# Performance work log

Measured on AMD Instinct MI355X. Metric: run time of the kernel, lower is better.

The kernel has to match this reference:

```python
import jax, jax.numpy as jnp
import numpy as np

E = 512   # embed_size
H = 8     # num_heads
D = E // H
N = 4
T = 2048


def quantize(x, b, e):
    # fake-quant: scale by 2^e, clamp to signed b-bit range, floor, dequant
    s = jnp.exp2(e)
    lo = -jnp.exp2(b - 1.0)
    hi = jnp.exp2(b - 1.0) - 1.0
    return jnp.floor(jnp.clip(x / s, lo, hi)) * s


def setup_inputs() -> dict:
    key = jax.random.key(0)
    ks = jax.random.split(key, 8)
    f = lambda k, shape: jax.random.normal(k, shape, dtype=jnp.float32)
    w = 1.0 / np.sqrt(E)  # ~ torch Linear init scale
    return {
        "values": f(ks[0], (N, T, E)),
        "keys": f(ks[1], (N, T, E)),
        "query": f(ks[2], (N, T, E)),
        "Wq": f(ks[3], (E, E)) * w, "bq": jnp.zeros((E,), jnp.float32),
        "Wk": f(ks[4], (E, E)) * w, "bk": jnp.zeros((E,), jnp.float32),
        "Wv": f(ks[5], (E, E)) * w, "bv": jnp.zeros((E,), jnp.float32),
        "Wo": f(ks[6], (E, E)) * w, "bo": jnp.zeros((E,), jnp.float32),
        "b_param": jnp.float32(8.0),
        "e_param": jnp.float32(0.0),
    }


def reference(values, keys, query, Wq, bq, Wk, bk, Wv, bv, Wo, bo, b_param, e_param):
    n, t, emb = query.shape
    d = emb // H
    # linear projections (torch Linear: x @ W^T + b), split heads -> [N,H,T,D]
    q = (query @ Wq.T + bq).reshape(n, t, H, d).transpose(0, 2, 1, 3)
    k = (keys @ Wk.T + bk).reshape(n, t, H, d).transpose(0, 2, 1, 3)
    v = (values @ Wv.T + bv).reshape(n, t, H, d).transpose(0, 2, 1, 3)
    b = jnp.clip(b_param, 1.0, 8.0)
    q = quantize(q, b, e_param)
    k = quantize(k, b, e_param)
    v = quantize(v, b, e_param)
    # NOTE: source scales by sqrt(embed_size), not sqrt(head_dim)
    energy = jnp.einsum('nhqd,nhkd->nhqk', q, k) / jnp.sqrt(jnp.float32(emb))
    attn = jax.nn.softmax(energy, axis=-1)
    out = jnp.einsum('nhqk,nhkd->nhqd', attn, v)
    out = out.transpose(0, 2, 1, 3).reshape(n, t, emb)
    return out @ Wo.T + bo
```

## Files before the change

kernel.cpp:

```cpp
#include <hip/hip_runtime.h>
#include <hip/hip_bf16.h>
#include <hip/hip_fp16.h>
#include <cstdint>
#include <cstddef>


typedef __attribute__((ext_vector_type(8))) _Float16 f16x8;
typedef __attribute__((ext_vector_type(2))) __fp16 hf16x2;
typedef __attribute__((ext_vector_type(16))) float f32x16;
typedef __attribute__((ext_vector_type(4))) unsigned u32x4;
typedef unsigned short u16;

#define EL  4194304
#define WEL 262144

static __device__ __forceinline__ u16 f2h(float x) {
  _Float16 h = (_Float16)x;
  return __builtin_bit_cast(u16, h);
}
static __device__ __forceinline__ unsigned pkh2(float a, float b) {
  hf16x2 p = __builtin_amdgcn_cvt_pkrtz(a, b);
  return __builtin_bit_cast(unsigned, p);
}
static __device__ __forceinline__ void gl_lds16(const void* g, void* l) {
  __builtin_amdgcn_global_load_lds(
      (__attribute__((address_space(1))) void*)g,
      (__attribute__((address_space(3))) void*)l, 16, 0, 0);
}

struct PrepAllArgs { const float* src[7]; };

__global__ __launch_bounds__(256) void prep_all_kernel(PrepAllArgs a,
                                                       u16* __restrict__ dst)
{
  const int i = blockIdx.x * 256 + threadIdx.x;
  const float* src; int off;
  if (i < 3145728) {
    const int m = i >> 20; off = i & 1048575;
    src = (m == 0) ? a.src[0] : (m == 1) ? a.src[1] : a.src[2];
  } else {
    const int j = i - 3145728; const int w = j >> 16; off = j & 65535;
    src = (w == 0) ? a.src[3] : (w == 1) ? a.src[4]
        : (w == 2) ? a.src[5] : a.src[6];
  }
  const float4 v = ((const float4*)src)[off];
  ushort4 o;
  o.x = f2h(v.x); o.y = f2h(v.y); o.z = f2h(v.z); o.w = f2h(v.w);
  ((ushort4*)dst)[i] = o;
}

struct ProjArgs {
  const u16* X[3]; const u16* W[3]; const float* bias[3];
  u16* dst[3]; int trans[3];
};

__global__ __launch_bounds__(256, 3) void proj_kernel(ProjArgs args,
    const float* __restrict__ bparam, const float* __restrict__ eparam)
{
  __shared__ u16 sm[17408];
  u16* const As = sm;
  u16* const Bs = sm + 8192;

  const int z = blockIdx.z;
  const u16* __restrict__ X = args.X[z];
  const u16* __restrict__ W = args.W[z];
  const float* __restrict__ bias = args.bias[z];
  u16* __restrict__ dst = args.dst[z];
  const int trans = args.trans[z];

  const int tid  = threadIdx.x;
  const int lane = tid & 63;
  const int wave = tid >> 6;
  const int lam  = lane & 31;
  const int hl   = lane >> 5;
  const int wm   = wave & 1;
  const int wn   = wave >> 1;
  const int mbase = blockIdx.x * 128;
  const int nbase = blockIdx.y * 128;

  const int srow = tid >> 3;
  const int sj   = (tid & 7) ^ (srow & 7);
  const u16* gA = X + (size_t)(mbase + srow) * 512 + sj * 8;
  const u16* gB = W + (size_t)(nbase + srow) * 512 + sj * 8;

  int offA[2][4], offB[2][4];
#pragma unroll
  for (int f = 0; f < 2; ++f)
#pragma unroll
    for (int kk = 0; kk < 4; ++kk) {
      const int c = 2 * kk + hl;
      const int m = wm * 64 + f * 32 + lam;
      offA[f][kk] = m * 128 + ((c ^ (m & 7)) * 16);
      const int nn = wn * 64 + f * 32 + lam;
      offB[f][kk] = nn * 128 + ((c ^ (nn & 7)) * 16);
    }

  f32x16 acc[2][2];
#pragma unroll
  for (int a = 0; a < 2; ++a)
#pragma unroll
    for (int b = 0; b < 2; ++b)
#pragma unroll
      for (int i = 0; i < 16; ++i) acc[a][b][i] = 0.f;

  for (int kt = 0; kt < 512; kt += 64) {
    __syncthreads();
#pragma unroll
    for (int t = 0; t < 4; ++t) {
      gl_lds16(gA + kt + t * 32 * 512, (char*)As + tid * 16 + t * 4096);
      gl_lds16(gB + kt + t * 32 * 512, (char*)Bs + tid * 16 + t * 4096);
    }
    __syncthreads();

    f16x8 fA[2][4], fB[2][4];
#pragma unroll
    for (int f = 0; f < 2; ++f)
#pragma unroll
      for (int kk = 0; kk < 4; ++kk) {
        fA[f][kk] = *(const f16x8*)((const char*)As + offA[f][kk]);
        fB[f][kk] = *(const f16x8*)((const char*)Bs + offB[f][kk]);
      }
#pragma unroll
    for (int mf = 0; mf < 2; ++mf)
#pragma unroll
      for (int nf = 0; nf < 2; ++nf)
#pragma unroll
        for (int kk = 0; kk < 4; ++kk)
          acc[mf][nf] = __builtin_amdgcn_mfma_f32_32x32x16_f16(
              fA[mf][kk], fB[nf][kk], acc[mf][nf], 0, 0, 0);
  }

  const float bq   = fminf(fmaxf(bparam[0], 1.0f), 8.0f);
  const float e    = eparam[0];
  const float s    = exp2f(e);
  const float invs = exp2f(-e);
  const float qlo  = -exp2f(bq - 1.0f);
  const float qhi  = exp2f(bq - 1.0f) - 1.0f;
  const int nidx = mbase >> 11;
  const int tb   = mbase & 2047;
  const int hb   = nbase >> 6;

  if (!trans) {
#pragma unroll
    for (int mf = 0; mf < 2; ++mf)
#pragma unroll
      for (int nf = 0; nf < 2; ++nf)
#pragma unroll
        for (int reg = 0; reg < 16; ++reg) {
          int col = wn * 64 + nf * 32 + lam;
          int row = wm * 64 + mf * 32 + (reg & 3) + 8 * (reg >> 2) + 4 * hl;
          float v = acc[mf][nf][reg] + bias[nbase + col];
          float qv = floorf(fminf(fmaxf(v * invs, qlo), qhi)) * s;
          dst[((size_t)(nidx * 8 + hb + (col >> 6)) * 2048 + tb + row) * 64 +
              (col & 63)] = f2h(qv);
        }
  } else {
    __syncthreads();
#pragma unroll
    for (int mf = 0; mf < 2; ++mf)
#pragma unroll
      for (int nf = 0; nf < 2; ++nf)
#pragma unroll
        for (int reg = 0; reg < 16; ++reg) {
          int col = wn * 64 + nf * 32 + lam;
          int row = wm * 64 + mf * 32 + (reg & 3) + 8 * (reg >> 2) + 4 * hl;
          float v = acc[mf][nf][reg] + bias[nbase + col];
          float qv = floorf(fminf(fmaxf(v * invs, qlo), qhi)) * s;
          sm[col * 136 + row] = f2h(qv);
        }
    __syncthreads();
    const int r = tid >> 1, half = tid & 1;
    const u16* sp = sm + r * 136 + half * 64;
    u16* gp = dst + ((size_t)(nidx * 8 + hb + (r >> 6)) * 64 + (r & 63)) * 2048 +
              tb + half * 64;
#pragma unroll
    for (int i = 0; i < 8; ++i)
      *(uint4*)(gp + i * 8) = *(const uint4*)(sp + i * 8);
  }
}

__global__ __launch_bounds__(256, 2) void attn_kernel(
    const u16* __restrict__ qbuf, const u16* __restrict__ kbuf,
    const u16* __restrict__ vtbuf, u16* __restrict__ ctx)
{
  __shared__ u16 sm[35328];
  char* const smc = (char*)sm;

  const int tid  = threadIdx.x;
  const int wave = tid >> 6;
  const int lane = tid & 63;
  const int lam  = lane & 31;
  const int hl   = lane >> 5;
  const int qt = blockIdx.x, hd = blockIdx.y, n = blockIdx.z;
  const int nh = n * 8 + hd;
  const int qbase = qt * 64;

  const u16* Qp = qbuf + ((size_t)nh * 2048 + qbase) * 64;
  const u16* Kp = kbuf + (size_t)nh * 131072;
  const u16* Vp = vtbuf + (size_t)nh * 131072;

  f16x8 qf[2][4];
#pragma unroll
  for (int qb = 0; qb < 2; ++qb)
#pragma unroll
    for (int dk = 0; dk < 4; ++dk)
      qf[qb][dk] = *(const f16x8*)(Qp + (qb * 32 + lam) * 64 + dk * 16 + hl * 8);

  const float sc = (float)(1.4426950408889634 / 22.627416997969522);

  const int r0 = tid >> 3;
  const int j0 = (tid & 7) ^ (r0 & 7);
  const u16* gK0 = Kp + (size_t)r0 * 64 + j0 * 8;
  const u16* gK1 = Kp + (size_t)(r0 + 32) * 64 + j0 * 8;
  const u16* gV0 = Vp + (size_t)r0 * 2048 + j0 * 8;
  const u16* gV1 = Vp + (size_t)(r0 + 32) * 2048 + j0 * 8;

  int offK[2][4], offV[2][4];
#pragma unroll
  for (int kf = 0; kf < 2; ++kf)
#pragma unroll
    for (int dk = 0; dk < 4; ++dk)
      offK[kf][dk] = wave * 8192 + (kf * 32 + lam) * 128 +
                     (((2 * dk + hl) ^ (lam & 7)) * 16);
#pragma unroll
  for (int nf = 0; nf < 2; ++nf)
#pragma unroll
    for (int kk = 0; kk < 4; ++kk)
      offV[nf][kk] = 32768 + wave * 8192 + (nf * 32 + lam) * 128 +
                     (((2 * kk + hl) ^ (lam & 7)) * 16);

  float l_acc[2] = {0.f, 0.f};
  f32x16 O[2][2];
#pragma unroll
  for (int a = 0; a < 2; ++a)
#pragma unroll
    for (int b = 0; b < 2; ++b)
#pragma unroll
      for (int i = 0; i < 16; ++i) O[a][b][i] = 0.f;

  for (int kt = 0; kt < 2048; kt += 256) {
    __syncthreads();
#pragma unroll
    for (int wt = 0; wt < 4; ++wt) {
      const size_t ko = (size_t)(kt + wt * 64) * 64;
      const int    vo = kt + wt * 64;
      gl_lds16(gK0 + ko, smc + wt * 8192 + tid * 16);
      gl_lds16(gK1 + ko, smc + wt * 8192 + tid * 16 + 4096);
      gl_lds16(gV0 + vo, smc + 32768 + wt * 8192 + tid * 16);
      gl_lds16(gV1 + vo, smc + 32768 + wt * 8192 + tid * 16 + 4096);
    }
    __syncthreads();

#pragma unroll
    for (int kf = 0; kf < 2; ++kf) {
      f16x8 Kf[4], Vf[2][2];
#pragma unroll
      for (int dk = 0; dk < 4; ++dk)
        Kf[dk] = *(const f16x8*)(smc + offK[kf][dk]);
#pragma unroll
      for (int nf = 0; nf < 2; ++nf)
#pragma unroll
        for (int kkl = 0; kkl < 2; ++kkl)
          Vf[nf][kkl] = *(const f16x8*)(smc + offV[nf][2 * kf + kkl]);

#pragma unroll
      for (int qb = 0; qb < 2; ++qb) {
        f32x16 S;
#pragma unroll
        for (int i = 0; i < 16; ++i) S[i] = 0.f;
#pragma unroll
        for (int dk = 0; dk < 4; ++dk)
          S = __builtin_amdgcn_mfma_f32_32x32x16_f16(Kf[dk], qf[qb][dk],
                                                     S, 0, 0, 0);
        unsigned pk[4][2];
#pragma unroll
        for (int gh = 0; gh < 4; ++gh) {
          float p0 = __builtin_amdgcn_exp2f(S[4 * gh + 0] * sc);
          float p1 = __builtin_amdgcn_exp2f(S[4 * gh + 1] * sc);
          float p2 = __builtin_amdgcn_exp2f(S[4 * gh + 2] * sc);
          float p3 = __builtin_amdgcn_exp2f(S[4 * gh + 3] * sc);
          l_acc[qb] += (p0 + p1) + (p2 + p3);
          pk[gh][0] = pkh2(p0, p1);
          pk[gh][1] = pkh2(p2, p3);
        }
        f16x8 pfrag[2];
#pragma unroll
        for (int kkl = 0; kkl < 2; ++kkl) {
          unsigned s0 = hl ? pk[2 * kkl][0] : pk[2 * kkl + 1][0];
          unsigned s1 = hl ? pk[2 * kkl][1] : pk[2 * kkl + 1][1];
          unsigned o0 = hl ? pk[2 * kkl + 1][0] : pk[2 * kkl][0];
          unsigned o1 = hl ? pk[2 * kkl + 1][1] : pk[2 * kkl][1];
          unsigned rr0 = (unsigned)__shfl_xor((int)s0, 32);
          unsigned rr1 = (unsigned)__shfl_xor((int)s1, 32);
          u32x4 f;
          f[0] = hl ? rr0 : o0;
          f[1] = hl ? rr1 : o1;
          f[2] = hl ? o0 : rr0;
          f[3] = hl ? o1 : rr1;
          pfrag[kkl] = __builtin_bit_cast(f16x8, f);
        }
#pragma unroll
        for (int nf = 0; nf < 2; ++nf)
#pragma unroll
          for (int kkl = 0; kkl < 2; ++kkl)
            O[qb][nf] = __builtin_amdgcn_mfma_f32_32x32x16_f16(
                pfrag[kkl], Vf[nf][kkl], O[qb][nf], 0, 0, 0);
      }
    }
  }

#pragma unroll
  for (int qb = 0; qb < 2; ++qb) l_acc[qb] += __shfl_xor(l_acc[qb], 32);
  __syncthreads();
  float* lred = (float*)(smc + 69632);
  if (hl == 0) {
    lred[wave * 64 + lam]      = l_acc[0];
    lred[wave * 64 + 32 + lam] = l_acc[1];
  }
  float* Ow = (float*)(smc + wave * 17408);
#pragma unroll
  for (int qb = 0; qb < 2; ++qb)
#pragma unroll
    for (int nf = 0; nf < 2; ++nf)
#pragma unroll
      for (int r = 0; r < 16; ++r) {
        int qrow = qb * 32 + (r & 3) + 8 * (r >> 2) + 4 * hl;
        Ow[qrow * 68 + nf * 32 + lam] = O[qb][nf][r];
      }
  __syncthreads();

  const int q  = tid >> 2;
  const int d4 = (tid & 3) * 64;
  float acc[16];
  {
    const float4 v0 = *(const float4*)(smc + q * 272 + d4);
    const float4 v1 = *(const float4*)(smc + q * 272 + d4 + 16);
    const float4 v2 = *(const float4*)(smc + q * 272 + d4 + 32);
    const float4 v3 = *(const float4*)(smc + q * 272 + d4 + 48);
    acc[0]=v0.x; acc[1]=v0.y; acc[2]=v0.z; acc[3]=v0.w;
    acc[4]=v1.x; acc[5]=v1.y; acc[6]=v1.z; acc[7]=v1.w;
    acc[8]=v2.x; acc[9]=v2.y; acc[10]=v2.z; acc[11]=v2.w;
    acc[12]=v3.x; acc[13]=v3.y; acc[14]=v3.z; acc[15]=v3.w;
  }
#pragma unroll
  for (int w = 1; w < 4; ++w) {
    const char* b = smc + w * 17408 + q * 272 + d4;
    const float4 v0 = *(const float4*)(b);
    const float4 v1 = *(const float4*)(b + 16);
    const float4 v2 = *(const float4*)(b + 32);
    const float4 v3 = *(const float4*)(b + 48);
    acc[0]+=v0.x; acc[1]+=v0.y; acc[2]+=v0.z; acc[3]+=v0.w;
    acc[4]+=v1.x; acc[5]+=v1.y; acc[6]+=v1.z; acc[7]+=v1.w;
    acc[8]+=v2.x; acc[9]+=v2.y; acc[10]+=v2.z; acc[11]+=v2.w;
    acc[12]+=v3.x; acc[13]+=v3.y; acc[14]+=v3.z; acc[15]+=v3.w;
  }
  const float lsum = lred[q] + lred[64 + q] + lred[128 + q] + lred[192 + q];
  const float rinv = 1.0f / lsum;
  unsigned outp[8];
#pragma unroll
  for (int i = 0; i < 8; ++i)
    outp[i] = pkh2(acc[2 * i] * rinv, acc[2 * i + 1] * rinv);
  u16* cp = ctx + ((size_t)n * 2048 + qbase + q) * 512 + hd * 64 + (tid & 3) * 16;
  *(uint4*)cp       = *(const uint4*)&outp[0];
  *(uint4*)(cp + 8) = *(const uint4*)&outp[4];
}

__global__ __launch_bounds__(256) void outproj_kernel(
    const u16* __restrict__ ctxb, const u16* __restrict__ Wof,
    const float* __restrict__ bias, float* __restrict__ out)
{
  __shared__ u16 sm[12288];
  u16* const As = sm;
  u16* const Bs = sm + 4096;

  const int tid  = threadIdx.x;
  const int lane = tid & 63;
  const int wave = tid >> 6;
  const int lam  = lane & 31;
  const int hl   = lane >> 5;
  const int wm   = wave & 1;
  const int wn   = wave >> 1;
  const int mbase = blockIdx.x * 64;
  const int nbase = blockIdx.y * 128;

  const int srow = tid >> 3;
  const int sj   = (tid & 7) ^ (srow & 7);
  const u16* gA = ctxb + (size_t)(mbase + srow) * 512 + sj * 8;
  const u16* gB = Wof  + (size_t)(nbase + srow) * 512 + sj * 8;

  int offA[4], offB[2][4];
#pragma unroll
  for (int kk = 0; kk < 4; ++kk) {
    const int c = 2 * kk + hl;
    const int m = wm * 32 + lam;
    offA[kk] = m * 128 + ((c ^ (m & 7)) * 16);
#pragma unroll
    for (int f = 0; f < 2; ++f) {
      const int nn = wn * 64 + f * 32 + lam;
      offB[f][kk] = nn * 128 + ((c ^ (nn & 7)) * 16);
    }
  }

  f32x16 acc[2];
#pragma unroll
  for (int a = 0; a < 2; ++a)
#pragma unroll
    for (int i = 0; i < 16; ++i) acc[a][i] = 0.f;

  for (int kt = 0; kt < 512; kt += 64) {
    __syncthreads();
#pragma unroll
    for (int t = 0; t < 2; ++t)
      gl_lds16(gA + kt + t * 32 * 512, (char*)As + tid * 16 + t * 4096);
#pragma unroll
    for (int t = 0; t < 4; ++t)
      gl_lds16(gB + kt + t * 32 * 512, (char*)Bs + tid * 16 + t * 4096);
    __syncthreads();

    f16x8 fA[4], fB[2][4];
#pragma unroll
    for (int kk = 0; kk < 4; ++kk) {
      fA[kk] = *(const f16x8*)((const char*)As + offA[kk]);
#pragma unroll
      for (int f = 0; f < 2; ++f)
        fB[f][kk] = *(const f16x8*)((const char*)Bs + offB[f][kk]);
    }
#pragma unroll
    for (int nf = 0; nf < 2; ++nf)
#pragma unroll
      for (int kk = 0; kk < 4; ++kk)
        acc[nf] = __builtin_amdgcn_mfma_f32_32x32x16_f16(
            fA[kk], fB[nf][kk], acc[nf], 0, 0, 0);
  }

#pragma unroll
  for (int nf = 0; nf < 2; ++nf)
#pragma unroll
    for (int reg = 0; reg < 16; ++reg) {
      int col = nbase + wn * 64 + nf * 32 + lam;
      int row = mbase + wm * 32 + (reg & 3) + 8 * (reg >> 2) + 4 * hl;
      out[(size_t)row * 512 + col] = acc[nf][reg] + bias[col];
    }
}

extern "C" void kernel_launch(void* const* d_in, const int* in_sizes, int n_in,
                              void* d_out, int out_size, void* d_ws, size_t ws_size,
                              hipStream_t stream) {
  (void)in_sizes; (void)n_in; (void)out_size; (void)ws_size;
  const float* values = (const float*)d_in[0];
  const float* keys   = (const float*)d_in[1];
  const float* query  = (const float*)d_in[2];
  const float* Wq = (const float*)d_in[3];  const float* bq = (const float*)d_in[4];
  const float* Wk = (const float*)d_in[5];  const float* bk = (const float*)d_in[6];
  const float* Wv = (const float*)d_in[7];  const float* bv = (const float*)d_in[8];
  const float* Wo = (const float*)d_in[9];  const float* bo = (const float*)d_in[10];
  const float* bp = (const float*)d_in[11]; const float* ep = (const float*)d_in[12];

  u16* ws    = (u16*)d_ws;
  u16* qbuf  = ws;
  u16* kbuf  = ws + (size_t)EL;
  u16* vtbuf = ws + (size_t)2 * EL;
  u16* ctx   = ws + (size_t)3 * EL;
  u16* xwf   = ws + (size_t)4 * EL;

  PrepAllArgs pa;
  pa.src[0] = query; pa.src[1] = keys; pa.src[2] = values;
  pa.src[3] = Wq; pa.src[4] = Wk; pa.src[5] = Wv; pa.src[6] = Wo;
  prep_all_kernel<<<13312, 256, 0, stream>>>(pa, xwf);

  const float* Bsrc[3] = {bq, bk, bv};
  u16* Dst[3] = {qbuf, kbuf, vtbuf};
  ProjArgs a;
  for (int m = 0; m < 3; ++m) {
    a.X[m] = xwf + (size_t)m * EL;
    a.W[m] = xwf + (size_t)3 * EL + (size_t)m * WEL;
    a.bias[m] = Bsrc[m]; a.dst[m] = Dst[m]; a.trans[m] = (m == 2);
  }
  proj_kernel<<<dim3(64, 4, 3), 256, 0, stream>>>(a, bp, ep);

  attn_kernel<<<dim3(32, 8, 4), 256, 0, stream>>>(qbuf, kbuf, vtbuf, ctx);
  outproj_kernel<<<dim3(128, 4), 256, 0, stream>>>(
      ctx, xwf + (size_t)3 * EL + (size_t)3 * WEL, bo, (float*)d_out);
}
```

Baseline: 194.2 us.

## Pre-swizzle K/V tiles in projection and pipeline per-wave async loads in attention

The projection kernel now writes K and V^T in a tiled, XOR-swizzled layout that matches the attention kernel's LDS fragment order. Each attention wave can then stream its own contiguous 32-key K/V chunks straight into private LDS with direct global-to-LDS loads. The loads are double-buffered using vmcnt waits instead of block-wide __syncthreads, which removes barrier stalls and overlaps loading with MFMA work. LDS use drops, and the final cross-wave reduction is split into two halves to fit the smaller buffer. The cost is fragile hand-written waitcnt sequencing and a layout coupling between the two kernels.

```diff
diff --git a/kernel.cpp b/kernel.cpp
--- a/kernel.cpp
+++ b/kernel.cpp
@@ -66,7 +66,7 @@
   const u16* __restrict__ W = args.W[z];
   const float* __restrict__ bias = args.bias[z];
   u16* __restrict__ dst = args.dst[z];
-  const int trans = args.trans[z];
+  const int mode = args.trans[z];
 
   const int tid  = threadIdx.x;
   const int lane = tid & 63;
@@ -140,7 +140,7 @@
   const int tb   = mbase & 2047;
   const int hb   = nbase >> 6;
 
-  if (!trans) {
+  if (mode == 0) {
 #pragma unroll
     for (int mf = 0; mf < 2; ++mf)
 #pragma unroll
@@ -154,6 +154,23 @@
           dst[((size_t)(nidx * 8 + hb + (col >> 6)) * 2048 + tb + row) * 64 +
               (col & 63)] = f2h(qv);
         }
+  } else if (mode == 1) {
+#pragma unroll
+    for (int mf = 0; mf < 2; ++mf)
+#pragma unroll
+      for (int nf = 0; nf < 2; ++nf)
+#pragma unroll
+        for (int reg = 0; reg < 16; ++reg) {
+          int col = wn * 64 + nf * 32 + lam;
+          int row = wm * 64 + mf * 32 + (reg & 3) + 8 * (reg >> 2) + 4 * hl;
+          float v = acc[mf][nf][reg] + bias[nbase + col];
+          float qv = floorf(fminf(fmaxf(v * invs, qlo), qhi)) * s;
+          const int t = tb + row;
+          const int d = col & 63;
+          dst[(size_t)(nidx * 8 + hb + (col >> 6)) * 131072 +
+              (t >> 5) * 2048 + (t & 31) * 64 + (((d >> 3) ^ (t & 7)) << 3) +
+              (d & 7)] = f2h(qv);
+        }
   } else {
     __syncthreads();
 #pragma unroll
@@ -171,11 +188,15 @@
     __syncthreads();
     const int r = tid >> 1, half = tid & 1;
     const u16* sp = sm + r * 136 + half * 64;
-    u16* gp = dst + ((size_t)(nidx * 8 + hb + (r >> 6)) * 64 + (r & 63)) * 2048 +
-              tb + half * 64;
-#pragma unroll
-    for (int i = 0; i < 8; ++i)
-      *(uint4*)(gp + i * 8) = *(const uint4*)(sp + i * 8);
+    const int d = r & 63;
+    const int dsw = d & 3;
+    u16* const gp0 = dst + (size_t)(nidx * 8 + hb + (r >> 6)) * 131072;
+#pragma unroll
+    for (int i = 0; i < 8; ++i) {
+      const int t = tb + half * 64 + i * 8;
+      *(uint4*)(gp0 + (t >> 5) * 2048 + d * 32 +
+                ((((t >> 3) & 3) ^ dsw) << 3)) = *(const uint4*)(sp + i * 8);
+    }
   }
 }
 
@@ -183,7 +204,7 @@
     const u16* __restrict__ qbuf, const u16* __restrict__ kbuf,
     const u16* __restrict__ vtbuf, u16* __restrict__ ctx)
 {
-  __shared__ u16 sm[35328];
+  __shared__ u16 sm[25088];
   char* const smc = (char*)sm;
 
   const int tid  = threadIdx.x;
@@ -196,8 +217,9 @@
   const int qbase = qt * 64;
 
   const u16* Qp = qbuf + ((size_t)nh * 2048 + qbase) * 64;
-  const u16* Kp = kbuf + (size_t)nh * 131072;
-  const u16* Vp = vtbuf + (size_t)nh * 131072;
+  const u16* gK = kbuf  + (size_t)nh * 131072 + wave * 2048 + lane * 8;
+  const u16* gV = vtbuf + (size_t)nh * 131072 + wave * 2048 + lane * 8;
+  char* const kvb = smc + wave * 12288;
 
   f16x8 qf[2][4];
 #pragma unroll
@@ -205,29 +227,36 @@
 #pragma unroll
     for (int dk = 0; dk < 4; ++dk)
       qf[qb][dk] = *(const f16x8*)(Qp + (qb * 32 + lam) * 64 + dk * 16 + hl * 8);
+#pragma unroll
+  for (int qb = 0; qb < 2; ++qb)
+#pragma unroll
+    for (int dk = 0; dk < 4; ++dk)
+      asm volatile("" :: "v"(qf[qb][dk]));
+
+  auto stage4 = [&](const u16* src, char* dstb) {
+#pragma unroll
+    for (int r = 0; r < 4; ++r)
+      gl_lds16(src + r * 512, dstb + r * 1024 + lane * 16);
+  };
+
+  stage4(gK,        kvb);
+  stage4(gV,        kvb + 8192);
+  stage4(gK + 8192, kvb + 4096);
+
+  int offK[4];
+#pragma unroll
+  for (int dk = 0; dk < 4; ++dk)
+    offK[dk] = lam * 128 + (((2 * dk + hl) ^ (lam & 7)) << 4);
+  int offV[2][2];
+#pragma unroll
+  for (int nf = 0; nf < 2; ++nf)
+#pragma unroll
+    for (int kkl = 0; kkl < 2; ++kkl) {
+      const int d = nf * 32 + lam;
+      offV[nf][kkl] = 8192 + d * 64 + (((2 * kkl + hl) ^ (d & 3)) << 4);
+    }
 
   const float sc = (float)(1.4426950408889634 / 22.627416997969522);
-
-  const int r0 = tid >> 3;
-  const int j0 = (tid & 7) ^ (r0 & 7);
-  const u16* gK0 = Kp + (size_t)r0 * 64 + j0 * 8;
-  const u16* gK1 = Kp + (size_t)(r0 + 32) * 64 + j0 * 8;
-  const u16* gV0 = Vp + (size_t)r0 * 2048 + j0 * 8;
-  const u16* gV1 = Vp + (size_t)(r0 + 32) * 2048 + j0 * 8;
-
-  int offK[2][4], offV[2][4];
-#pragma unroll
-  for (int kf = 0; kf < 2; ++kf)
-#pragma unroll
-    for (int dk = 0; dk < 4; ++dk)
-      offK[kf][dk] = wave * 8192 + (kf * 32 + lam) * 128 +
-                     (((2 * dk + hl) ^ (lam & 7)) * 16);
-#pragma unroll
-  for (int nf = 0; nf < 2; ++nf)
-#pragma unroll
-    for (int kk = 0; kk < 4; ++kk)
-      offV[nf][kk] = 32768 + wave * 8192 + (nf * 32 + lam) * 128 +
-                     (((2 * kk + hl) ^ (lam & 7)) * 16);
 
   float l_acc[2] = {0.f, 0.f};
   f32x16 O[2][2];
@@ -238,131 +267,124 @@
 #pragma unroll
       for (int i = 0; i < 16; ++i) O[a][b][i] = 0.f;
 
-  for (int kt = 0; kt < 2048; kt += 256) {
-    __syncthreads();
-#pragma unroll
-    for (int wt = 0; wt < 4; ++wt) {
-      const size_t ko = (size_t)(kt + wt * 64) * 64;
-      const int    vo = kt + wt * 64;
-      gl_lds16(gK0 + ko, smc + wt * 8192 + tid * 16);
-      gl_lds16(gK1 + ko, smc + wt * 8192 + tid * 16 + 4096);
-      gl_lds16(gV0 + vo, smc + 32768 + wt * 8192 + tid * 16);
-      gl_lds16(gV1 + vo, smc + 32768 + wt * 8192 + tid * 16 + 4096);
-    }
-    __syncthreads();
-
-#pragma unroll
-    for (int kf = 0; kf < 2; ++kf) {
-      f16x8 Kf[4], Vf[2][2];
+  for (int t = 0; t < 16; ++t) {
+    char* const kb = kvb + (t & 1) * 4096;
+    asm volatile("s_waitcnt vmcnt(8)" ::: "memory");
+    f16x8 Kf[4];
+#pragma unroll
+    for (int dk = 0; dk < 4; ++dk)
+      Kf[dk] = *(const f16x8*)(kb + offK[dk]);
+
+    f16x8 pfrag[2][2];
+#pragma unroll
+    for (int qb = 0; qb < 2; ++qb) {
+      f32x16 S;
+#pragma unroll
+      for (int i = 0; i < 16; ++i) S[i] = 0.f;
 #pragma unroll
       for (int dk = 0; dk < 4; ++dk)
-        Kf[dk] = *(const f16x8*)(smc + offK[kf][dk]);
+        S = __builtin_amdgcn_mfma_f32_32x32x16_f16(Kf[dk], qf[qb][dk],
+                                                   S, 0, 0, 0);
+      unsigned pk[4][2];
+#pragma unroll
+      for (int gh = 0; gh < 4; ++gh) {
+        float p0 = __builtin_amdgcn_exp2f(S[4 * gh + 0] * sc);
+        float p1 = __builtin_amdgcn_exp2f(S[4 * gh + 1] * sc);
+        float p2 = __builtin_amdgcn_exp2f(S[4 * gh + 2] * sc);
+        float p3 = __builtin_amdgcn_exp2f(S[4 * gh + 3] * sc);
+        l_acc[qb] += (p0 + p1) + (p2 + p3);
+        pk[gh][0] = pkh2(p0, p1);
+        pk[gh][1] = pkh2(p2, p3);
+      }
+#pragma unroll
+      for (int kkl = 0; kkl < 2; ++kkl) {
+        unsigned s0 = hl ? pk[2 * kkl][0] : pk[2 * kkl + 1][0];
+        unsigned s1 = hl ? pk[2 * kkl][1] : pk[2 * kkl + 1][1];
+        unsigned o0 = hl ? pk[2 * kkl + 1][0] : pk[2 * kkl][0];
+        unsigned o1 = hl ? pk[2 * kkl + 1][1] : pk[2 * kkl][1];
+        unsigned rr0 = (unsigned)__shfl_xor((int)s0, 32);
+        unsigned rr1 = (unsigned)__shfl_xor((int)s1, 32);
+        u32x4 f;
+        f[0] = hl ? rr0 : o0;
+        f[1] = hl ? rr1 : o1;
+        f[2] = hl ? o0 : rr0;
+        f[3] = hl ? o1 : rr1;
+        pfrag[qb][kkl] = __builtin_bit_cast(f16x8, f);
+      }
+    }
+
+    asm volatile("s_waitcnt vmcnt(4)" ::: "memory");
+    f16x8 Vf[2][2];
+#pragma unroll
+    for (int nf = 0; nf < 2; ++nf)
+#pragma unroll
+      for (int kkl = 0; kkl < 2; ++kkl)
+        Vf[nf][kkl] = *(const f16x8*)(kvb + offV[nf][kkl]);
+#pragma unroll
+    for (int qb = 0; qb < 2; ++qb)
 #pragma unroll
       for (int nf = 0; nf < 2; ++nf)
 #pragma unroll
         for (int kkl = 0; kkl < 2; ++kkl)
-          Vf[nf][kkl] = *(const f16x8*)(smc + offV[nf][2 * kf + kkl]);
-
-#pragma unroll
-      for (int qb = 0; qb < 2; ++qb) {
-        f32x16 S;
-#pragma unroll
-        for (int i = 0; i < 16; ++i) S[i] = 0.f;
-#pragma unroll
-        for (int dk = 0; dk < 4; ++dk)
-          S = __builtin_amdgcn_mfma_f32_32x32x16_f16(Kf[dk], qf[qb][dk],
-                                                     S, 0, 0, 0);
-        unsigned pk[4][2];
-#pragma unroll
-        for (int gh = 0; gh < 4; ++gh) {
-          float p0 = __builtin_amdgcn_exp2f(S[4 * gh + 0] * sc);
-          float p1 = __builtin_amdgcn_exp2f(S[4 * gh + 1] * sc);
-          float p2 = __builtin_amdgcn_exp2f(S[4 * gh + 2] * sc);
-          float p3 = __builtin_amdgcn_exp2f(S[4 * gh + 3] * sc);
-          l_acc[qb] += (p0 + p1) + (p2 + p3);
-          pk[gh][0] = pkh2(p0, p1);
-          pk[gh][1] = pkh2(p2, p3);
-        }
-        f16x8 pfrag[2];
-#pragma unroll
-        for (int kkl = 0; kkl < 2; ++kkl) {
-          unsigned s0 = hl ? pk[2 * kkl][0] : pk[2 * kkl + 1][0];
-          unsigned s1 = hl ? pk[2 * kkl][1] : pk[2 * kkl + 1][1];
-          unsigned o0 = hl ? pk[2 * kkl + 1][0] : pk[2 * kkl][0];
-          unsigned o1 = hl ? pk[2 * kkl + 1][1] : pk[2 * kkl][1];
-          unsigned rr0 = (unsigned)__shfl_xor((int)s0, 32);
-          unsigned rr1 = (unsigned)__shfl_xor((int)s1, 32);
-          u32x4 f;
-          f[0] = hl ? rr0 : o0;
-          f[1] = hl ? rr1 : o1;
-          f[2] = hl ? o0 : rr0;
-          f[3] = hl ? o1 : rr1;
-          pfrag[kkl] = __builtin_bit_cast(f16x8, f);
-        }
-#pragma unroll
-        for (int nf = 0; nf < 2; ++nf)
-#pragma unroll
-          for (int kkl = 0; kkl < 2; ++kkl)
-            O[qb][nf] = __builtin_amdgcn_mfma_f32_32x32x16_f16(
-                pfrag[kkl], Vf[nf][kkl], O[qb][nf], 0, 0, 0);
-      }
-    }
-  }
-
+          O[qb][nf] = __builtin_amdgcn_mfma_f32_32x32x16_f16(
+              pfrag[qb][kkl], Vf[nf][kkl], O[qb][nf], 0, 0, 0);
+
+    asm volatile("s_waitcnt lgkmcnt(0)" ::: "memory");
+    stage4(gV + ((t + 1) & 15) * 8192, kvb + 8192);
+    stage4(gK + ((t + 2) & 15) * 8192, kvb + (t & 1) * 4096);
+  }
+
+  asm volatile("s_waitcnt vmcnt(0)" ::: "memory");
 #pragma unroll
   for (int qb = 0; qb < 2; ++qb) l_acc[qb] += __shfl_xor(l_acc[qb], 32);
-  __syncthreads();
-  float* lred = (float*)(smc + 69632);
+  float* lred = (float*)(smc + 49152);
   if (hl == 0) {
     lred[wave * 64 + lam]      = l_acc[0];
     lred[wave * 64 + 32 + lam] = l_acc[1];
   }
-  float* Ow = (float*)(smc + wave * 17408);
-#pragma unroll
-  for (int qb = 0; qb < 2; ++qb)
+  __syncthreads();
+
+  const int q  = tid >> 3;
+  const int dc = (tid & 7) * 8;
+#pragma unroll
+  for (int qb = 0; qb < 2; ++qb) {
+    float* Ow = (float*)(smc + wave * 8704);
 #pragma unroll
     for (int nf = 0; nf < 2; ++nf)
 #pragma unroll
       for (int r = 0; r < 16; ++r) {
-        int qrow = qb * 32 + (r & 3) + 8 * (r >> 2) + 4 * hl;
+        const int qrow = (r & 3) + 8 * (r >> 2) + 4 * hl;
         Ow[qrow * 68 + nf * 32 + lam] = O[qb][nf][r];
       }
-  __syncthreads();
-
-  const int q  = tid >> 2;
-  const int d4 = (tid & 3) * 64;
-  float acc[16];
-  {
-    const float4 v0 = *(const float4*)(smc + q * 272 + d4);
-    const float4 v1 = *(const float4*)(smc + q * 272 + d4 + 16);
-    const float4 v2 = *(const float4*)(smc + q * 272 + d4 + 32);
-    const float4 v3 = *(const float4*)(smc + q * 272 + d4 + 48);
-    acc[0]=v0.x; acc[1]=v0.y; acc[2]=v0.z; acc[3]=v0.w;
-    acc[4]=v1.x; acc[5]=v1.y; acc[6]=v1.z; acc[7]=v1.w;
-    acc[8]=v2.x; acc[9]=v2.y; acc[10]=v2.z; acc[11]=v2.w;
-    acc[12]=v3.x; acc[13]=v3.y; acc[14]=v3.z; acc[15]=v3.w;
-  }
-#pragma unroll
-  for (int w = 1; w < 4; ++w) {
-    const char* b = smc + w * 17408 + q * 272 + d4;
-    const float4 v0 = *(const float4*)(b);
-    const float4 v1 = *(const float4*)(b + 16);
-    const float4 v2 = *(const float4*)(b + 32);
-    const float4 v3 = *(const float4*)(b + 48);
-    acc[0]+=v0.x; acc[1]+=v0.y; acc[2]+=v0.z; acc[3]+=v0.w;
-    acc[4]+=v1.x; acc[5]+=v1.y; acc[6]+=v1.z; acc[7]+=v1.w;
-    acc[8]+=v2.x; acc[9]+=v2.y; acc[10]+=v2.z; acc[11]+=v2.w;
-    acc[12]+=v3.x; acc[13]+=v3.y; acc[14]+=v3.z; acc[15]+=v3.w;
-  }
-  const float lsum = lred[q] + lred[64 + q] + lred[128 + q] + lred[192 + q];
-  const float rinv = 1.0f / lsum;
-  unsigned outp[8];
-#pragma unroll
-  for (int i = 0; i < 8; ++i)
-    outp[i] = pkh2(acc[2 * i] * rinv, acc[2 * i + 1] * rinv);
-  u16* cp = ctx + ((size_t)n * 2048 + qbase + q) * 512 + hd * 64 + (tid & 3) * 16;
-  *(uint4*)cp       = *(const uint4*)&outp[0];
-  *(uint4*)(cp + 8) = *(const uint4*)&outp[4];
+    __syncthreads();
+    float a[8];
+    {
+      const char* b = smc + q * 272 + dc * 4;
+      const float4 v0 = *(const float4*)b;
+      const float4 v1 = *(const float4*)(b + 16);
+      a[0] = v0.x; a[1] = v0.y; a[2] = v0.z; a[3] = v0.w;
+      a[4] = v1.x; a[5] = v1.y; a[6] = v1.z; a[7] = v1.w;
+    }
+#pragma unroll
+    for (int w = 1; w < 4; ++w) {
+      const char* b = smc + w * 8704 + q * 272 + dc * 4;
+      const float4 v0 = *(const float4*)b;
+      const float4 v1 = *(const float4*)(b + 16);
+      a[0] += v0.x; a[1] += v0.y; a[2] += v0.z; a[3] += v0.w;
+      a[4] += v1.x; a[5] += v1.y; a[6] += v1.z; a[7] += v1.w;
+    }
+    const float lsum = lred[qb * 32 + q] + lred[64 + qb * 32 + q] +
+                       lred[128 + qb * 32 + q] + lred[192 + qb * 32 + q];
+    const float rinv = 1.0f / lsum;
+    unsigned outp[4];
+#pragma unroll
+    for (int i = 0; i < 4; ++i)
+      outp[i] = pkh2(a[2 * i] * rinv, a[2 * i + 1] * rinv);
+    u16* cp = ctx + ((size_t)n * 2048 + qbase + qb * 32 + q) * 512 +
+              hd * 64 + dc;
+    *(uint4*)cp = *(const uint4*)outp;
+    if (qb == 0) __syncthreads();
+  }
 }
 
 __global__ __launch_bounds__(256) void outproj_kernel(
@@ -474,7 +496,7 @@
   for (int m = 0; m < 3; ++m) {
     a.X[m] = xwf + (size_t)m * EL;
     a.W[m] = xwf + (size_t)3 * EL + (size_t)m * WEL;
-    a.bias[m] = Bsrc[m]; a.dst[m] = Dst[m]; a.trans[m] = (m == 2);
+    a.bias[m] = Bsrc[m]; a.dst[m] = Dst[m]; a.trans[m] = m;
   }
   proj_kernel<<<dim3(64, 4, 3), 256, 0, stream>>>(a, bp, ep);
 
```

New measurement: 193.3 us. About the same (-0.5%).
